# Optimization experiments

Hardware: AMD Instinct MI355X
Metric: run time of the kernel (lower is better)

The kernel has to match this reference:

```python
import jax, jax.numpy as jnp
import numpy as np

L = 4          # n_layers
A = 4          # aspect heads: causal, intentional, temporal, normative
D = 1024       # d_model
DK = D // A    # 256
S = 3072
NE, NA = 1536, 1024  # n_events, n_agents (norms = S - NE - NA)
EPS = 1e-5


def _layernorm(x, g, b):
    mu = jnp.mean(x, axis=-1, keepdims=True)
    var = jnp.mean(jnp.square(x - mu), axis=-1, keepdims=True)
    return g * (x - mu) * jax.lax.rsqrt(var + EPS) + b


def setup_inputs() -> dict:
    key = jax.random.key(0)
    ks = jax.random.split(key, 12)
    s = 0.02
    return {
        "hidden": jax.random.normal(ks[0], (1, S, D), jnp.float32),
        "Wq": jax.random.normal(ks[1], (L, D, D), jnp.float32) * s,
        "bq": jnp.zeros((L, D), jnp.float32),
        "Wk": jax.random.normal(ks[2], (L, D, D), jnp.float32) * s,
        "bk": jnp.zeros((L, D), jnp.float32),
        "Wv": jax.random.normal(ks[3], (L, D, D), jnp.float32) * s,
        "bv": jnp.zeros((L, D), jnp.float32),
        "Wh": jax.random.normal(ks[4], (L, A, D, DK), jnp.float32) * s,
        "bh": jnp.zeros((L, A, DK), jnp.float32),
        "Wo": jax.random.normal(ks[5], (L, D, D), jnp.float32) * s,
        "bo": jnp.zeros((L, D), jnp.float32),
        "g1": jnp.ones((L, D), jnp.float32),
        "b1n": jnp.zeros((L, D), jnp.float32),
        "g2": jnp.ones((L, D), jnp.float32),
        "b2n": jnp.zeros((L, D), jnp.float32),
        "Wf1": jax.random.normal(ks[6], (L, D, 2 * D), jnp.float32) * s,
        "bf1": jnp.zeros((L, 2 * D), jnp.float32),
        "Wf2": jax.random.normal(ks[7], (L, 2 * D, D), jnp.float32) * s,
        "bf2": jnp.zeros((L, D), jnp.float32),
        "Whead": jax.random.normal(ks[8], (4, D), jnp.float32) * s,  # guilt, causation, intention, harm
        "bhead": jnp.zeros((4,), jnp.float32),
        "n_events": NE,
        "n_agents": NA,
    }


def reference(hidden, Wq, bq, Wk, bk, Wv, bv, Wh, bh, Wo, bo,
              g1, b1n, g2, b2n, Wf1, bf1, Wf2, bf2, Whead, bhead,
              n_events, n_agents):
    scale = 1.0 / np.sqrt(DK).astype(np.float32)
    h = hidden  # [B, S, D]
    for l in range(L):
        Q = h @ Wq[l] + bq[l]
        K = h @ Wk[l] + bk[l]
        V = h @ Wv[l] + bv[l]
        # per-aspect projections: [B, A, S, DK]
        Qh = jnp.einsum('bsd,ade->base', Q, Wh[l]) + bh[l][None, :, None, :]
        Kh = jnp.einsum('bsd,ade->base', K, Wh[l]) + bh[l][None, :, None, :]
        Vh = jnp.einsum('bsd,ade->base', V, Wh[l]) + bh[l][None, :, None, :]
        scores = jnp.einsum('base,bate->bast', Qh, Kh) * scale  # [B, A, S, S]
        attn = jax.nn.softmax(scores, axis=-1)  # dropout = identity (eval)
        ctx = jnp.einsum('bast,bate->base', attn, Vh)  # [B, A, S, DK]
        B = ctx.shape[0]
        ctx = ctx.transpose(0, 2, 1, 3).reshape(B, S, D)  # concat aspect heads
        attn_out = ctx @ Wo[l] + bo[l]
        h = _layernorm(h + attn_out, g1[l], b1n[l])
        ffn = jax.nn.relu(h @ Wf1[l] + bf1[l]) @ Wf2[l] + bf2[l]
        h = _layernorm(h + ffn, g2[l], b2n[l])
    event_h = h[:, :n_events, :]
    agent_h = h[:, n_events:n_events + n_agents, :]
    guilt = agent_h @ Whead[0] + bhead[0]      # [B, n_agents]
    causation = agent_h @ Whead[1] + bhead[1]
    intention = agent_h @ Whead[2] + bhead[2]
    harm = event_h @ Whead[3] + bhead[3]       # [B, n_events]
    return jnp.concatenate([guilt, causation, intention, harm], axis=-1)
```

## Files before the change

### kernel.cpp

```cpp
#include <hip/hip_runtime.h>
#include <cstdint>

typedef unsigned short u16;
typedef __bf16  bf16x8 __attribute__((ext_vector_type(8)));
typedef float   f32x4  __attribute__((ext_vector_type(4)));
typedef unsigned short u16x4 __attribute__((ext_vector_type(4)));
typedef unsigned short u16x8 __attribute__((ext_vector_type(8)));

#define S_LEN 3072
#define DMODEL 1024

__device__ __forceinline__ float bf2f(u16 u){ return __uint_as_float(((unsigned)u) << 16); }
__device__ __forceinline__ u16 f2bf(float f){
    unsigned u = __float_as_uint(f);
    return (u16)((u + 0x7fffu + ((u >> 16) & 1u)) >> 16);
}
__device__ __forceinline__ u16 cvld(const void* p, long i, int mode){
    return mode ? f2bf(((const float*)p)[i]) : ((const u16*)p)[i];
}

__device__ __forceinline__ void async16(const void* g, void* l){
    __builtin_amdgcn_global_load_lds(
        (const __attribute__((address_space(1))) unsigned int*)g,
        (__attribute__((address_space(3))) unsigned int*)l, 16, 0, 0);
}

__global__ void sniff_kernel(const u16* __restrict__ x, int* __restrict__ flag)
{
    __shared__ int r[256];
    int tid = threadIdx.x, w = 0;
    for (int j = tid; j < 4096; j += 256){
        int e = (x[j] >> 7) & 0xFF;
        if (e < 90 || e > 140) w++;
    }
    r[tid] = w; __syncthreads();
    for (int s = 128; s > 0; s >>= 1){ if (tid < s) r[tid] += r[tid + s]; __syncthreads(); }
    if (tid == 0){ flag[0] = (r[0] > 256) ? 1 : 0; flag[1] = 0; }
}

__global__ __launch_bounds__(256)
void gemm_scores(const u16* __restrict__ A, int lda,
                 const u16* __restrict__ B, int ldb,
                 u16* __restrict__ C, int ldc,
                 float* __restrict__ rowSums,
                 int K, long aBS, long bBS, long cBS)
{
    __shared__ __align__(16) u16 smem[2 * 128 * 64];
    u16* Abuf = smem;
    u16* Bbuf = smem + 128 * 64;
    const int tid  = threadIdx.x;
    const int lane = tid & 63, wid = tid >> 6;
    const int wm = wid >> 1, wn = wid & 1;
    const int quad = lane >> 4, lr = lane & 15;
    const int bat = blockIdx.z;

    A += (long)bat * aBS + (long)blockIdx.x * 128 * lda;
    B += (long)bat * bBS + (long)blockIdx.y * 128 * ldb;

    f32x4 zero = {0.f, 0.f, 0.f, 0.f};
    f32x4 acc[4][4];
#pragma unroll
    for (int i = 0; i < 4; i++)
#pragma unroll
        for (int j = 0; j < 4; j++) acc[i][j] = zero;

    int um[4], ukq[4];
#pragma unroll
    for (int i = 0; i < 4; i++){
        int u = i * 256 + tid;
        um[i]  = u >> 3;
        ukq[i] = u & 7;
    }

    const int kTiles = K >> 6;
    for (int kt = 0; kt < kTiles; ++kt){
        const int k0 = kt << 6;
        __syncthreads();
#pragma unroll
        for (int i = 0; i < 4; i++)
            async16(A + (long)um[i] * lda + k0 + ukq[i] * 8, Abuf + (i * 256 + tid) * 8);
#pragma unroll
        for (int i = 0; i < 4; i++)
            async16(B + (long)um[i] * ldb + k0 + ukq[i] * 8, Bbuf + (i * 256 + tid) * 8);
        __syncthreads();
#pragma unroll
        for (int ks = 0; ks < 2; ++ks){
            bf16x8 af[4], bfg[4];
#pragma unroll
            for (int t = 0; t < 4; t++){
                int m  = wm * 64 + t * 16 + lr;
                af[t]  = *(const bf16x8*)(Abuf + (m * 8 + ks * 4 + quad) * 8);
                int n  = wn * 64 + t * 16 + lr;
                bfg[t] = *(const bf16x8*)(Bbuf + (n * 8 + ks * 4 + quad) * 8);
            }
#pragma unroll
            for (int mt = 0; mt < 4; mt++)
#pragma unroll
                for (int nt = 0; nt < 4; nt++)
                    acc[mt][nt] = __builtin_amdgcn_mfma_f32_16x16x32_bf16(
                        af[mt], bfg[nt], acc[mt][nt], 0, 0, 0);
        }
    }

    const int rowBase = blockIdx.x * 128 + wm * 64;
    const int colBase = blockIdx.y * 128 + wn * 64;
    const float scale = 0.0625f;
    float* scw = (float*)smem + (size_t)wid * (16 * 68);
    const int row_l = lane >> 2, cq = lane & 3;

#pragma unroll
    for (int mt = 0; mt < 4; ++mt){
        __syncthreads();
#pragma unroll
        for (int nt = 0; nt < 4; nt++)
#pragma unroll
            for (int r = 0; r < 4; r++)
                scw[(quad * 4 + r) * 68 + nt * 16 + lr] = acc[mt][nt][r];
        __syncthreads();
        float vals[16];
#pragma unroll
        for (int j = 0; j < 4; j++)
            *(f32x4*)(vals + j * 4) = *(const f32x4*)(scw + row_l * 68 + cq * 16 + j * 4);
        float rs = 0.f;
        u16x8 pk0, pk1;
#pragma unroll
        for (int i = 0; i < 16; i++){
            float e = __expf(vals[i] * scale);
            rs += e;
            if (i < 8) pk0[i] = f2bf(e); else pk1[i - 8] = f2bf(e);
        }
        rs += __shfl_xor(rs, 1, 64);
        rs += __shfl_xor(rs, 2, 64);
        int row_g = rowBase + mt * 16 + row_l;
        if (cq == 0) atomicAdd(&rowSums[(long)bat * S_LEN + row_g], rs);
        u16* cp = C + (long)bat * cBS + (long)row_g * ldc + colBase + cq * 16;
        *(u16x8*)cp       = pk0;
        *(u16x8*)(cp + 8) = pk1;
    }
}

template<int SPLIT, int MODE>
__global__ __launch_bounds__(256)
void gemm64(const u16* __restrict__ A, int lda,
            const u16* __restrict__ B, int ldb,
            void* __restrict__ Cv, int ldc,
            const u16* __restrict__ bias,
            int K, long aBS, long bBS, long cBS, long pStride)
{
    __shared__ __align__(16) u16 smem[64 * 64 + 128 * 64];
    u16* Abuf = smem;
    u16* Bbuf = smem + 64 * 64;
    const int tid  = threadIdx.x;
    const int lane = tid & 63, wid = tid >> 6;
    const int quad = lane >> 4, lr = lane & 15;

    const int z   = blockIdx.z;
    const int bat = z / SPLIT;
    const int sp  = z % SPLIT;
    const int kLen = K / SPLIT;

    A += (long)bat * aBS + (long)blockIdx.x * 64 * lda + (long)sp * kLen;
    B += (long)bat * bBS + (long)blockIdx.y * 128 * ldb + (long)sp * kLen;

    f32x4 zero = {0.f, 0.f, 0.f, 0.f};
    f32x4 acc[4][2];
#pragma unroll
    for (int i = 0; i < 4; i++){ acc[i][0] = zero; acc[i][1] = zero; }

    const int kTiles = kLen >> 6;
    for (int kt = 0; kt < kTiles; ++kt){
        const int k0 = kt << 6;
        __syncthreads();
#pragma unroll
        for (int i = 0; i < 2; i++){
            int u = i * 256 + tid;
            async16(A + (long)(u >> 3) * lda + k0 + (u & 7) * 8, Abuf + u * 8);
        }
#pragma unroll
        for (int i = 0; i < 4; i++){
            int u = i * 256 + tid;
            async16(B + (long)(u >> 3) * ldb + k0 + (u & 7) * 8, Bbuf + u * 8);
        }
        __syncthreads();
#pragma unroll
        for (int ks = 0; ks < 2; ++ks){
            bf16x8 af[4], bfg[2];
#pragma unroll
            for (int t = 0; t < 4; t++){
                int m  = t * 16 + lr;
                af[t]  = *(const bf16x8*)(Abuf + (m * 8 + ks * 4 + quad) * 8);
            }
#pragma unroll
            for (int t = 0; t < 2; t++){
                int n  = wid * 32 + t * 16 + lr;
                bfg[t] = *(const bf16x8*)(Bbuf + (n * 8 + ks * 4 + quad) * 8);
            }
#pragma unroll
            for (int mt = 0; mt < 4; mt++)
#pragma unroll
                for (int nt = 0; nt < 2; nt++)
                    acc[mt][nt] = __builtin_amdgcn_mfma_f32_16x16x32_bf16(
                        af[mt], bfg[nt], acc[mt][nt], 0, 0, 0);
        }
    }

    const int rowBase = blockIdx.x * 64;
    const int colBase = blockIdx.y * 128 + wid * 32;
    const int slabw = colBase >> 10;

    if (MODE == 1 && slabw == 2){
        u16* scw = smem + (size_t)wid * (32 * 72);
        __syncthreads();
#pragma unroll
        for (int nt = 0; nt < 2; nt++){
            float bv2 = bf2f(bias[colBase + nt * 16 + lr]);
#pragma unroll
            for (int mt = 0; mt < 4; mt++){
                u16x4 pk;
#pragma unroll
                for (int r = 0; r < 4; r++) pk[r] = f2bf(acc[mt][nt][r] + bv2);
                *(u16x4*)(scw + (nt * 16 + lr) * 72 + mt * 16 + quad * 4) = pk;
            }
        }
        __syncthreads();
        const int e_l = lane >> 1, sh = lane & 1;
        const int e_g = (colBase & 1023) + e_l;
        u16* dst = (u16*)Cv + (long)2 * S_LEN * DMODEL + (long)e_g * S_LEN
                 + rowBase + sh * 32;
#pragma unroll
        for (int j = 0; j < 4; j++)
            *(u16x8*)(dst + j * 8) = *(const u16x8*)(scw + e_l * 72 + sh * 32 + j * 8);
        return;
    }

    float* scw = (float*)smem + (size_t)wid * (16 * 36);
    const int row_l = lane >> 2, cq = lane & 3;
#pragma unroll
    for (int mt = 0; mt < 4; ++mt){
        __syncthreads();
#pragma unroll
        for (int nt = 0; nt < 2; nt++)
#pragma unroll
            for (int r = 0; r < 4; r++)
                scw[(quad * 4 + r) * 36 + nt * 16 + lr] = acc[mt][nt][r];
        __syncthreads();
        f32x4 a = *(const f32x4*)(scw + row_l * 36 + cq * 8);
        f32x4 b = *(const f32x4*)(scw + row_l * 36 + cq * 8 + 4);
        const int row_g = rowBase + mt * 16 + row_l;
        const int colg  = colBase + cq * 8;
        if (SPLIT > 1){
            float* P = (float*)Cv + (long)sp * pStride + (long)bat * cBS;
            *(f32x4*)(P + (long)row_g * ldc + colg)     = a;
            *(f32x4*)(P + (long)row_g * ldc + colg + 4) = b;
        } else {
            float bv[8];
            if (bias){
                u16x8 bb = *(const u16x8*)(bias + colg);
#pragma unroll
                for (int i = 0; i < 8; i++) bv[i] = bf2f(bb[i]);
            } else {
#pragma unroll
                for (int i = 0; i < 8; i++) bv[i] = 0.f;
            }
            u16x8 pk;
#pragma unroll
            for (int i = 0; i < 8; i++){
                float v = (i < 4 ? a[i] : b[i - 4]) + bv[i];
                if (MODE == 2) v = fmaxf(v, 0.f);
                pk[i] = f2bf(v);
            }
            long idx;
            if (MODE == 1) idx = ((long)slabw * S_LEN + row_g) * DMODEL + (colg & 1023);
            else           idx = (long)bat * cBS + (long)row_g * ldc + colg;
            *(u16x8*)((u16*)Cv + idx) = pk;
        }
    }
}

__global__ __launch_bounds__(256)
void wprep(const int* __restrict__ flag, int l,
           const void* Wo, const void* Wf1, const void* Wf2, const void* Wh,
           const void* Wq, const void* Wk, const void* Wv,
           u16* __restrict__ WoT, u16* __restrict__ Wf1T,
           u16* __restrict__ Wf2T, u16* __restrict__ WhT,
           u16* __restrict__ Wcat)
{
    const int mode = *flag;
    const int z = blockIdx.x;
    const int tx = threadIdx.x, ty = threadIdx.y;

    if (z >= 6144){
        int t = ty * 32 + tx;
        long base = (long)(z - 6144) * 2048;
#pragma unroll
        for (int j = 0; j < 8; j++){
            long g = base + j * 256 + t;
            int slab = (int)(g >> 20);
            long r = g & 1048575;
            const void* src = (slab == 0) ? Wq : (slab == 1) ? Wk : Wv;
            Wcat[g] = cvld(src, (long)l * 1048576 + r, mode);
        }
        return;
    }

    const void* in; u16* out; long ib; int R, C, rb, cb;
    if (z < 1024){
        in = Wo; out = WoT; ib = (long)l * 1048576; R = 1024; C = 1024;
        cb = z & 31; rb = z >> 5;
    } else if (z < 3072){
        int t = z - 1024;
        in = Wf1; out = Wf1T; ib = (long)l * 2097152; R = 1024; C = 2048;
        cb = t & 63; rb = t >> 6;
    } else if (z < 5120){
        int t = z - 3072;
        in = Wf2; out = Wf2T; ib = (long)l * 2097152; R = 2048; C = 1024;
        cb = t & 31; rb = t >> 5;
    } else {
        int t = z - 5120;
        int a = t >> 8, u = t & 255;
        in = Wh; out = WhT + (long)a * 262144;
        ib = (long)l * 1048576 + (long)a * 262144; R = 1024; C = 256;
        cb = u & 7; rb = u >> 3;
    }

    __shared__ u16 tbuf[32][34];
    int r0 = rb * 32, c0 = cb * 32;
#pragma unroll
    for (int j = 0; j < 4; j++){
        int r = r0 + ty + j * 8;
        tbuf[ty + j * 8][tx] = cvld(in, ib + (long)r * C + c0 + tx, mode);
    }
    __syncthreads();
#pragma unroll
    for (int j = 0; j < 4; j++){
        int c = c0 + ty + j * 8;
        out[(long)c * R + r0 + tx] = tbuf[tx][ty + j * 8];
    }
}

__global__ __launch_bounds__(256)
void init_h(const int* __restrict__ flag, const void* __restrict__ hin,
            float* __restrict__ h, u16* __restrict__ hbf)
{
    const int mode = *flag;
    long i = (long)blockIdx.x * 256 + threadIdx.x;
    u16 u = cvld(hin, i, mode);
    h[i]   = bf2f(u);
    hbf[i] = u;
}

__global__ __launch_bounds__(256)
void zero_sums(float* __restrict__ p)
{
    p[blockIdx.x * 256 + threadIdx.x] = 0.f;
}

#define OFF_BQKV 0
#define OFF_BH   12288
#define OFF_BO   16384
#define OFF_BF1  20480
#define OFF_BF2  28672
#define OFF_G1   32768
#define OFF_B1N  36864
#define OFF_G2   40960
#define OFF_B2N  45056
#define OFF_WHD  49152
#define OFF_BHD  53248
#define BIAS_TOT 53252

__global__ __launch_bounds__(256)
void cvt_biases(const int* __restrict__ flag,
                const void* bq, const void* bk, const void* bv, const void* bh,
                const void* bo, const void* bf1, const void* bf2,
                const void* g1, const void* b1n, const void* g2, const void* b2n,
                const void* whd, const void* bhd, u16* __restrict__ A)
{
    int i = blockIdx.x * 256 + threadIdx.x;
    if (i >= BIAS_TOT) return;
    const int mode = *flag;
    u16 v;
    if (i < OFF_BH){
        int l = i / 3072, r = i % 3072;
        const void* p = (r < 1024) ? bq : (r < 2048) ? bk : bv;
        v = cvld(p, (long)l * 1024 + (r & 1023), mode);
    }
    else if (i < OFF_BO)  v = cvld(bh,  i - OFF_BH, mode);
    else if (i < OFF_BF1) v = cvld(bo,  i - OFF_BO, mode);
    else if (i < OFF_BF2) v = cvld(bf1, i - OFF_BF1, mode);
    else if (i < OFF_G1)  v = cvld(bf2, i - OFF_BF2, mode);
    else if (i < OFF_B1N) v = cvld(g1,  i - OFF_G1, mode);
    else if (i < OFF_G2)  v = cvld(b1n, i - OFF_B1N, mode);
    else if (i < OFF_B2N) v = cvld(g2,  i - OFF_G2, mode);
    else if (i < OFF_WHD) v = cvld(b2n, i - OFF_B2N, mode);
    else if (i < OFF_BHD) v = cvld(whd, i - OFF_WHD, mode);
    else                  v = cvld(bhd, i - OFF_BHD, mode);
    A[i] = v;
}

__global__ __launch_bounds__(256)
void bias_combine(const u16* __restrict__ arena, const u16* __restrict__ WhT,
                  int l, u16* __restrict__ bqkvh)
{
    int i = blockIdx.x * 256 + threadIdx.x;
    int z = i >> 10, n = i & 1023;
    const u16* bz = arena + OFF_BQKV + l * 3072 + z * 1024;
    const u16* wr = WhT + (long)n * 1024;
    float s = bf2f(arena[OFF_BH + l * 1024 + n]);
    for (int d = 0; d < 1024; d += 8){
        bf16x8 w = *(const bf16x8*)(wr + d);
        bf16x8 b = *(const bf16x8*)(bz + d);
#pragma unroll
        for (int j = 0; j < 8; j++) s += (float)w[j] * (float)b[j];
    }
    bqkvh[i] = f2bf(s);
}

__device__ __forceinline__ float blockSum(float v, float* red){
    int lane = threadIdx.x & 63, wid = threadIdx.x >> 6;
#pragma unroll
    for (int o = 32; o > 0; o >>= 1) v += __shfl_down(v, o, 64);
    __syncthreads();
    if (lane == 0) red[wid] = v;
    __syncthreads();
    return red[0] + red[1] + red[2] + red[3];
}

__global__ __launch_bounds__(256)
void ln_fused(float* __restrict__ h, const float* __restrict__ parts, long pStride,
              int nparts, const u16* __restrict__ bias, u16* __restrict__ hbf,
              const u16* __restrict__ g, const u16* __restrict__ b)
{
    __shared__ float red[4];
    long base = (long)blockIdx.x * DMODEL;
    int tid = threadIdx.x;
    float v[4];
    float s = 0.f;
#pragma unroll
    for (int j = 0; j < 4; j++){
        int c = tid + j * 256;
        float x = bf2f(bias[c]);
        for (int sp = 0; sp < nparts; sp++) x += parts[(long)sp * pStride + base + c];
        float r = h[base + c] + x;
        v[j] = r; s += r;
    }
    float mu = blockSum(s, red) * (1.f / DMODEL);
    float s2 = 0.f;
#pragma unroll
    for (int j = 0; j < 4; j++){ float d = v[j] - mu; s2 += d * d; }
    float var = blockSum(s2, red) * (1.f / DMODEL);
    float inv = rsqrtf(var + 1e-5f);
#pragma unroll
    for (int j = 0; j < 4; j++){
        int c = tid + j * 256;
        float y = (v[j] - mu) * inv * bf2f(g[c]) + bf2f(b[c]);
        h[base + c]   = y;
        hbf[base + c] = f2bf(y);
    }
}

__global__ __launch_bounds__(256)
void reduce_div(const float* __restrict__ parts, long pStride, int nsplit,
                const float* __restrict__ l, u16* __restrict__ out)
{
    long i0 = ((long)blockIdx.x * 256 + threadIdx.x) * 4;
    int row  = (int)(i0 >> 10);
    int head = (int)((i0 & 1023) >> 8);
    float inv = 1.f / l[(long)head * S_LEN + row];
#pragma unroll
    for (int j = 0; j < 4; j++){
        long i = i0 + j;
        float s = 0.f;
        for (int sp = 0; sp < nsplit; sp++) s += parts[(long)sp * pStride + i];
        out[i] = f2bf(s * inv);
    }
}

__global__ __launch_bounds__(256)
void head_kernel(const int* __restrict__ flag, const float* __restrict__ h,
                 const u16* __restrict__ arena, const int* __restrict__ nePtr,
                 const int* __restrict__ naPtr, void* __restrict__ outp)
{
    __shared__ float red[4];
    int o = blockIdx.x;
    int ne = *nePtr, na = *naPtr;
    int widx, row;
    if (o < 3 * na){ widx = o / na; row = ne + o % na; }
    else           { widx = 3;      row = o - 3 * na; }
    int tid = threadIdx.x;
    const float* hr = h + (long)row * DMODEL;
    const u16*   w  = arena + OFF_WHD + widx * DMODEL;
    float s = 0.f;
#pragma unroll
    for (int j = 0; j < 4; j++){ int c = tid + j * 256; s += hr[c] * bf2f(w[c]); }
    s = blockSum(s, red);
    if (tid == 0){
        float r = s + bf2f(arena[OFF_BHD + widx]);
        if (*flag) ((float*)outp)[o] = r;
        else       ((u16*)outp)[o]   = f2bf(r);
    }
}

extern "C" void kernel_launch(void* const* d_in, const int* in_sizes, int n_in,
                              void* d_out, int out_size, void* d_ws, size_t ws_size,
                              hipStream_t stream)
{
    const void* hidden = d_in[0];
    const void* Wq  = d_in[1];  const void* bq  = d_in[2];
    const void* Wk  = d_in[3];  const void* bk  = d_in[4];
    const void* Wv  = d_in[5];  const void* bv  = d_in[6];
    const void* Wh  = d_in[7];  const void* bh  = d_in[8];
    const void* Wo  = d_in[9];  const void* bo  = d_in[10];
    const void* g1  = d_in[11]; const void* b1n = d_in[12];
    const void* g2  = d_in[13]; const void* b2n = d_in[14];
    const void* Wf1 = d_in[15]; const void* bf1 = d_in[16];
    const void* Wf2 = d_in[17]; const void* bf2 = d_in[18];
    const void* Whd = d_in[19]; const void* bhd = d_in[20];
    const int* nePtr = (const int*)d_in[21];
    const int* naPtr = (const int*)d_in[22];

    const long D = 1024, S = 3072, L = 4, DK = 256;

    char* ws = (char*)d_ws;
    size_t off = 0;
    auto alloc = [&](size_t bytes)->char*{
        char* p = ws + off;
        off = (off + bytes + 255) & ~(size_t)255;
        return p;
    };
    int*  flag   = (int*)alloc(256);
    u16*  barena = (u16*)alloc(BIAS_TOT * 2);
    u16*  bqkvh  = (u16*)alloc(3 * D * 2);
    float* rowSums = (float*)alloc(4 * S * 4);
    u16*  WhT    = (u16*)alloc(D * D * 2);
    u16*  WqkvhT = (u16*)alloc(3 * D * D * 2);
    u16*  WoT    = (u16*)alloc(D * D * 2);
    u16*  Wf1T   = (u16*)alloc(2 * D * D * 2);
    u16*  Wf2T   = (u16*)alloc(2 * D * D * 2);
    float* h     = (float*)alloc(S * D * 4);
    u16*  hbf    = (u16*)alloc(S * D * 2);
    u16*  qkvh   = (u16*)alloc(3 * S * D * 2);
    u16*  ctx    = (u16*)alloc(S * D * 2);
    size_t baseEnd = off;

    size_t reg4 = (size_t)4 * S * S * 2;
    size_t reg1 = (size_t)S * S * 2 + (size_t)S * 2 * D * 2;
    int HBv = (ws_size >= baseEnd + reg4 + 2 * (size_t)S * D * 4 + 4096) ? 4 : 1;
    char* regionB = alloc(HBv == 4 ? reg4 : reg1);
    size_t endB = off;
    size_t cp1 = (size_t)S * D * 4;
    int ctxSplit = (ws_size >= endB + 2 * cp1 + 4096) ? 2 : 1;
    float* ctxParts = (float*)alloc((size_t)ctxSplit * cp1);

    u16* scoresP = (u16*)regionB;
    u16* Wcat    = (u16*)regionB;
    float* woParts = (float*)regionB;
    u16* ffn1;
    float* f2Parts;
    if (HBv == 4){
        ffn1    = (u16*)regionB;
        f2Parts = (float*)(regionB + (size_t)S * 2 * D * 2);
    } else {
        ffn1    = (u16*)(regionB + (size_t)S * S * 2);
        f2Parts = (float*)ctxParts;
    }

    const long pSD = S * D;

    dim3 tb(32, 8);
    sniff_kernel<<<1, 256, 0, stream>>>((const u16*)hidden, flag);
    cvt_biases<<<(BIAS_TOT + 255) / 256, 256, 0, stream>>>(
        flag, bq, bk, bv, bh, bo, bf1, bf2, g1, b1n, g2, b2n, Whd, bhd, barena);
    init_h<<<(int)(S * D / 256), 256, 0, stream>>>(flag, hidden, h, hbf);

    for (int l = 0; l < L; ++l){
        wprep<<<7680, tb, 0, stream>>>(flag, l, Wo, Wf1, Wf2, Wh, Wq, Wk, Wv,
                                       WoT, Wf1T, Wf2T, WhT, Wcat);
        gemm64<1, 0><<<dim3(16, 8, 3), 256, 0, stream>>>(
            WhT, 1024, Wcat, 1024, WqkvhT, 1024, nullptr,
            1024, 0, (long)D * D, (long)D * D, 0);
        bias_combine<<<12, 256, 0, stream>>>(barena, WhT, l, bqkvh);

        gemm64<1, 1><<<dim3(48, 24, 1), 256, 0, stream>>>(
            hbf, 1024, WqkvhT, 1024, qkvh, 0, bqkvh,
            1024, 0, 0, 0, 0);

        zero_sums<<<48, 256, 0, stream>>>(rowSums);
        if (HBv == 4){
            gemm_scores<<<dim3(24, 24, 4), 256, 0, stream>>>(
                qkvh, 1024, qkvh + S * D, 1024, scoresP, (int)S,
                rowSums, (int)DK, DK, DK, (long)S * S);
            gemm64<2, 0><<<dim3(48, 2, 8), 256, 0, stream>>>(
                scoresP, (int)S, qkvh + 2 * S * D, (int)S,
                ctxParts, 1024, nullptr, (int)S,
                (long)S * S, (long)DK * S, DK, pSD);
        } else {
            for (int h0 = 0; h0 < 4; ++h0){
                gemm_scores<<<dim3(24, 24, 1), 256, 0, stream>>>(
                    qkvh + h0 * DK, 1024, qkvh + S * D + h0 * DK, 1024,
                    scoresP, (int)S, rowSums + h0 * S, (int)DK, 0, 0, 0);
                gemm64<2, 0><<<dim3(48, 2, 2), 256, 0, stream>>>(
                    scoresP, (int)S, qkvh + 2 * S * D + (long)h0 * DK * S, (int)S,
                    ctxParts + h0 * DK, 1024, nullptr, (int)S,
                    0, 0, 0, ctxSplit == 2 ? pSD : 0);
            }
        }
        reduce_div<<<3072, 256, 0, stream>>>(ctxParts, pSD, ctxSplit, rowSums, ctx);

        gemm64<2, 0><<<dim3(48, 8, 2), 256, 0, stream>>>(
            ctx, 1024, WoT, 1024, woParts, 1024, nullptr,
            1024, 0, 0, 0, pSD);
        ln_fused<<<3072, 256, 0, stream>>>(h, woParts, pSD, 2, barena + OFF_BO + l * D,
                                           hbf, barena + OFF_G1 + l * D, barena + OFF_B1N + l * D);
        gemm64<1, 2><<<dim3(48, 16, 1), 256, 0, stream>>>(
            hbf, 1024, Wf1T, 1024, ffn1, 2048, barena + OFF_BF1 + l * 2 * D,
            1024, 0, 0, 0, 0);
        gemm64<2, 0><<<dim3(48, 8, 2), 256, 0, stream>>>(
            ffn1, 2048, Wf2T, 2048, f2Parts, 1024, nullptr,
            2048, 0, 0, 0, pSD);
        ln_fused<<<3072, 256, 0, stream>>>(h, f2Parts, pSD, 2, barena + OFF_BF2 + l * D,
                                           hbf, barena + OFF_G2 + l * D, barena + OFF_B2N + l * D);
    }
    head_kernel<<<out_size, 256, 0, stream>>>(flag, h, barena, nePtr, naPtr, d_out);
}
```

Before: 1.366 ms.

## Fuse softmax normalization into PV GEMM, store split-K partials as bf16, trim barriers

The PV GEMM no longer uses split-K. It divides by the softmax row sums in its epilogue and writes bf16 context directly, which removes the reduce_div kernel and the fp32 context partial buffers. Row-sum zeroing moves into the wprep launch, and the split-K partials for Wo and FFN2 are now written as bf16 instead of fp32 to halve their traffic. Per-tile __syncthreads in the epilogues are reduced to a single barrier, since each wave uses its own scratch region. In exchange, the PV GEMM launches fewer blocks, and bf16 partials lose some precision before the layernorm sum.

```diff
diff --git a/kernel.cpp b/kernel.cpp
--- a/kernel.cpp
+++ b/kernel.cpp
@@ -108,15 +108,14 @@
     float* scw = (float*)smem + (size_t)wid * (16 * 68);
     const int row_l = lane >> 2, cq = lane & 3;
 
+    __syncthreads();
 #pragma unroll
     for (int mt = 0; mt < 4; ++mt){
-        __syncthreads();
 #pragma unroll
         for (int nt = 0; nt < 4; nt++)
 #pragma unroll
             for (int r = 0; r < 4; r++)
                 scw[(quad * 4 + r) * 68 + nt * 16 + lr] = acc[mt][nt][r];
-        __syncthreads();
         float vals[16];
 #pragma unroll
         for (int j = 0; j < 4; j++)
@@ -145,7 +144,8 @@
             const u16* __restrict__ B, int ldb,
             void* __restrict__ Cv, int ldc,
             const u16* __restrict__ bias,
-            int K, long aBS, long bBS, long cBS, long pStride)
+            int K, long aBS, long bBS, long cBS, long pStride,
+            const float* __restrict__ rs)
 {
     __shared__ __align__(16) u16 smem[64 * 64 + 128 * 64];
     u16* Abuf = smem;
@@ -208,9 +208,10 @@
     const int colBase = blockIdx.y * 128 + wid * 32;
     const int slabw = colBase >> 10;
 
+    __syncthreads();
+
     if (MODE == 1 && slabw == 2){
         u16* scw = smem + (size_t)wid * (32 * 72);
-        __syncthreads();
 #pragma unroll
         for (int nt = 0; nt < 2; nt++){
             float bv2 = bf2f(bias[colBase + nt * 16 + lr]);
@@ -222,7 +223,6 @@
                 *(u16x4*)(scw + (nt * 16 + lr) * 72 + mt * 16 + quad * 4) = pk;
             }
         }
-        __syncthreads();
         const int e_l = lane >> 1, sh = lane & 1;
         const int e_g = (colBase & 1023) + e_l;
         u16* dst = (u16*)Cv + (long)2 * S_LEN * DMODEL + (long)e_g * S_LEN
@@ -237,43 +237,39 @@
     const int row_l = lane >> 2, cq = lane & 3;
 #pragma unroll
     for (int mt = 0; mt < 4; ++mt){
-        __syncthreads();
 #pragma unroll
         for (int nt = 0; nt < 2; nt++)
 #pragma unroll
             for (int r = 0; r < 4; r++)
                 scw[(quad * 4 + r) * 36 + nt * 16 + lr] = acc[mt][nt][r];
-        __syncthreads();
         f32x4 a = *(const f32x4*)(scw + row_l * 36 + cq * 8);
         f32x4 b = *(const f32x4*)(scw + row_l * 36 + cq * 8 + 4);
         const int row_g = rowBase + mt * 16 + row_l;
         const int colg  = colBase + cq * 8;
-        if (SPLIT > 1){
-            float* P = (float*)Cv + (long)sp * pStride + (long)bat * cBS;
-            *(f32x4*)(P + (long)row_g * ldc + colg)     = a;
-            *(f32x4*)(P + (long)row_g * ldc + colg + 4) = b;
+        float inv = 1.f;
+        if (MODE == 3) inv = 1.f / rs[(long)bat * S_LEN + row_g];
+        float bv[8];
+        if (SPLIT == 1 && MODE != 3 && bias){
+            u16x8 bb = *(const u16x8*)(bias + colg);
+#pragma unroll
+            for (int i = 0; i < 8; i++) bv[i] = bf2f(bb[i]);
         } else {
-            float bv[8];
-            if (bias){
-                u16x8 bb = *(const u16x8*)(bias + colg);
-#pragma unroll
-                for (int i = 0; i < 8; i++) bv[i] = bf2f(bb[i]);
-            } else {
-#pragma unroll
-                for (int i = 0; i < 8; i++) bv[i] = 0.f;
-            }
-            u16x8 pk;
-#pragma unroll
-            for (int i = 0; i < 8; i++){
-                float v = (i < 4 ? a[i] : b[i - 4]) + bv[i];
-                if (MODE == 2) v = fmaxf(v, 0.f);
-                pk[i] = f2bf(v);
-            }
-            long idx;
-            if (MODE == 1) idx = ((long)slabw * S_LEN + row_g) * DMODEL + (colg & 1023);
-            else           idx = (long)bat * cBS + (long)row_g * ldc + colg;
-            *(u16x8*)((u16*)Cv + idx) = pk;
-        }
+#pragma unroll
+            for (int i = 0; i < 8; i++) bv[i] = 0.f;
+        }
+        u16x8 pk;
+#pragma unroll
+        for (int i = 0; i < 8; i++){
+            float v = (i < 4 ? a[i] : b[i - 4]) + bv[i];
+            if (MODE == 2) v = fmaxf(v, 0.f);
+            if (MODE == 3) v *= inv;
+            pk[i] = f2bf(v);
+        }
+        long idx;
+        if (SPLIT > 1)      idx = (long)sp * pStride + (long)bat * cBS + (long)row_g * ldc + colg;
+        else if (MODE == 1) idx = ((long)slabw * S_LEN + row_g) * DMODEL + (colg & 1023);
+        else                idx = (long)bat * cBS + (long)row_g * ldc + colg;
+        *(u16x8*)((u16*)Cv + idx) = pk;
     }
 }
 
@@ -283,12 +279,17 @@
            const void* Wq, const void* Wk, const void* Wv,
            u16* __restrict__ WoT, u16* __restrict__ Wf1T,
            u16* __restrict__ Wf2T, u16* __restrict__ WhT,
-           u16* __restrict__ Wcat)
+           u16* __restrict__ Wcat, float* __restrict__ rowSums)
 {
     const int mode = *flag;
     const int z = blockIdx.x;
     const int tx = threadIdx.x, ty = threadIdx.y;
 
+    if (z >= 7680){
+        int idx = (z - 7680) * 256 + ty * 32 + tx;
+        rowSums[idx] = 0.f;
+        return;
+    }
     if (z >= 6144){
         int t = ty * 32 + tx;
         long base = (long)(z - 6144) * 2048;
@@ -349,12 +350,6 @@
     hbf[i] = u;
 }
 
-__global__ __launch_bounds__(256)
-void zero_sums(float* __restrict__ p)
-{
-    p[blockIdx.x * 256 + threadIdx.x] = 0.f;
-}
-
 #define OFF_BQKV 0
 #define OFF_BH   12288
 #define OFF_BO   16384
@@ -426,7 +421,7 @@
 }
 
 __global__ __launch_bounds__(256)
-void ln_fused(float* __restrict__ h, const float* __restrict__ parts, long pStride,
+void ln_fused(float* __restrict__ h, const u16* __restrict__ parts, long pStride,
               int nparts, const u16* __restrict__ bias, u16* __restrict__ hbf,
               const u16* __restrict__ g, const u16* __restrict__ b)
 {
@@ -439,7 +434,7 @@
     for (int j = 0; j < 4; j++){
         int c = tid + j * 256;
         float x = bf2f(bias[c]);
-        for (int sp = 0; sp < nparts; sp++) x += parts[(long)sp * pStride + base + c];
+        for (int sp = 0; sp < nparts; sp++) x += bf2f(parts[(long)sp * pStride + base + c]);
         float r = h[base + c] + x;
         v[j] = r; s += r;
     }
@@ -455,23 +450,6 @@
         float y = (v[j] - mu) * inv * bf2f(g[c]) + bf2f(b[c]);
         h[base + c]   = y;
         hbf[base + c] = f2bf(y);
-    }
-}
-
-__global__ __launch_bounds__(256)
-void reduce_div(const float* __restrict__ parts, long pStride, int nsplit,
-                const float* __restrict__ l, u16* __restrict__ out)
-{
-    long i0 = ((long)blockIdx.x * 256 + threadIdx.x) * 4;
-    int row  = (int)(i0 >> 10);
-    int head = (int)((i0 & 1023) >> 8);
-    float inv = 1.f / l[(long)head * S_LEN + row];
-#pragma unroll
-    for (int j = 0; j < 4; j++){
-        long i = i0 + j;
-        float s = 0.f;
-        for (int sp = 0; sp < nsplit; sp++) s += parts[(long)sp * pStride + i];
-        out[i] = f2bf(s * inv);
     }
 }
 
@@ -544,24 +522,20 @@
 
     size_t reg4 = (size_t)4 * S * S * 2;
     size_t reg1 = (size_t)S * S * 2 + (size_t)S * 2 * D * 2;
-    int HBv = (ws_size >= baseEnd + reg4 + 2 * (size_t)S * D * 4 + 4096) ? 4 : 1;
+    int HBv = (ws_size >= baseEnd + reg4 + 4096) ? 4 : 1;
     char* regionB = alloc(HBv == 4 ? reg4 : reg1);
-    size_t endB = off;
-    size_t cp1 = (size_t)S * D * 4;
-    int ctxSplit = (ws_size >= endB + 2 * cp1 + 4096) ? 2 : 1;
-    float* ctxParts = (float*)alloc((size_t)ctxSplit * cp1);
 
     u16* scoresP = (u16*)regionB;
     u16* Wcat    = (u16*)regionB;
-    float* woParts = (float*)regionB;
+    u16* woParts = (u16*)regionB;
     u16* ffn1;
-    float* f2Parts;
+    u16* f2Parts;
     if (HBv == 4){
         ffn1    = (u16*)regionB;
-        f2Parts = (float*)(regionB + (size_t)S * 2 * D * 2);
+        f2Parts = (u16*)(regionB + (size_t)S * 2 * D * 2);
     } else {
         ffn1    = (u16*)(regionB + (size_t)S * S * 2);
-        f2Parts = (float*)ctxParts;
+        f2Parts = (u16*)regionB;
     }
 
     const long pSD = S * D;
@@ -573,50 +547,48 @@
     init_h<<<(int)(S * D / 256), 256, 0, stream>>>(flag, hidden, h, hbf);
 
     for (int l = 0; l < L; ++l){
-        wprep<<<7680, tb, 0, stream>>>(flag, l, Wo, Wf1, Wf2, Wh, Wq, Wk, Wv,
-                                       WoT, Wf1T, Wf2T, WhT, Wcat);
+        wprep<<<7728, tb, 0, stream>>>(flag, l, Wo, Wf1, Wf2, Wh, Wq, Wk, Wv,
+                                       WoT, Wf1T, Wf2T, WhT, Wcat, rowSums);
         gemm64<1, 0><<<dim3(16, 8, 3), 256, 0, stream>>>(
             WhT, 1024, Wcat, 1024, WqkvhT, 1024, nullptr,
-            1024, 0, (long)D * D, (long)D * D, 0);
+            1024, 0, (long)D * D, (long)D * D, 0, nullptr);
         bias_combine<<<12, 256, 0, stream>>>(barena, WhT, l, bqkvh);
 
         gemm64<1, 1><<<dim3(48, 24, 1), 256, 0, stream>>>(
             hbf, 1024, WqkvhT, 1024, qkvh, 0, bqkvh,
-            1024, 0, 0, 0, 0);
-
-        zero_sums<<<48, 256, 0, stream>>>(rowSums);
+            1024, 0, 0, 0, 0, nullptr);
+
         if (HBv == 4){
             gemm_scores<<<dim3(24, 24, 4), 256, 0, stream>>>(
                 qkvh, 1024, qkvh + S * D, 1024, scoresP, (int)S,
                 rowSums, (int)DK, DK, DK, (long)S * S);
-            gemm64<2, 0><<<dim3(48, 2, 8), 256, 0, stream>>>(
+            gemm64<1, 3><<<dim3(48, 2, 4), 256, 0, stream>>>(
                 scoresP, (int)S, qkvh + 2 * S * D, (int)S,
-                ctxParts, 1024, nullptr, (int)S,
-                (long)S * S, (long)DK * S, DK, pSD);
+                ctx, 1024, nullptr, (int)S,
+                (long)S * S, (long)DK * S, DK, 0, rowSums);
         } else {
             for (int h0 = 0; h0 < 4; ++h0){
                 gemm_scores<<<dim3(24, 24, 1), 256, 0, stream>>>(
                     qkvh + h0 * DK, 1024, qkvh + S * D + h0 * DK, 1024,
                     scoresP, (int)S, rowSums + h0 * S, (int)DK, 0, 0, 0);
-                gemm64<2, 0><<<dim3(48, 2, 2), 256, 0, stream>>>(
+                gemm64<1, 3><<<dim3(48, 2, 1), 256, 0, stream>>>(
                     scoresP, (int)S, qkvh + 2 * S * D + (long)h0 * DK * S, (int)S,
-                    ctxParts + h0 * DK, 1024, nullptr, (int)S,
-                    0, 0, 0, ctxSplit == 2 ? pSD : 0);
+                    ctx + h0 * DK, 1024, nullptr, (int)S,
+                    0, 0, 0, 0, rowSums + h0 * S);
             }
         }
-        reduce_div<<<3072, 256, 0, stream>>>(ctxParts, pSD, ctxSplit, rowSums, ctx);
 
         gemm64<2, 0><<<dim3(48, 8, 2), 256, 0, stream>>>(
             ctx, 1024, WoT, 1024, woParts, 1024, nullptr,
-            1024, 0, 0, 0, pSD);
+            1024, 0, 0, 0, pSD, nullptr);
         ln_fused<<<3072, 256, 0, stream>>>(h, woParts, pSD, 2, barena + OFF_BO + l * D,
                                            hbf, barena + OFF_G1 + l * D, barena + OFF_B1N + l * D);
         gemm64<1, 2><<<dim3(48, 16, 1), 256, 0, stream>>>(
             hbf, 1024, Wf1T, 1024, ffn1, 2048, barena + OFF_BF1 + l * 2 * D,
-            1024, 0, 0, 0, 0);
+            1024, 0, 0, 0, 0, nullptr);
         gemm64<2, 0><<<dim3(48, 8, 2), 256, 0, stream>>>(
             ffn1, 2048, Wf2T, 2048, f2Parts, 1024, nullptr,
-            2048, 0, 0, 0, pSD);
+            2048, 0, 0, 0, pSD, nullptr);
         ln_fused<<<3072, 256, 0, stream>>>(h, f2Parts, pSD, 2, barena + OFF_BF2 + l * D,
                                            hbf, barena + OFF_G2 + l * D, barena + OFF_B2N + l * D);
     }
```

Result: no change. 1.363 ms (-0.2%).
